# Kernel optimization log

Hardware: AMD Instinct MI355X
Metric: run time of the kernel (lower is better)

Reference implementation:

```python
import jax, jax.numpy as jnp
import numpy as np
import math

B, S, D, H = 2, 2048, 1024, 16
DH = D // H  # head_size = 64


def setup_inputs() -> dict:
    key = jax.random.key(0)
    ks = jax.random.split(key, 11)
    s = 0.02
    return {
        "queries": jax.random.normal(ks[0], (B, S, D), jnp.float32),
        "keys": jax.random.normal(ks[1], (B, S, D), jnp.float32),
        "values": jax.random.normal(ks[2], (B, S, D), jnp.float32),
        # nn.Linear weights: y = x @ W.T + b, W has shape (out, in)
        "W_Q": jax.random.normal(ks[3], (D, D), jnp.float32) * s,
        "b_Q": jax.random.normal(ks[4], (D,), jnp.float32) * s,
        "W_K": jax.random.normal(ks[5], (D, D), jnp.float32) * s,
        "b_K": jax.random.normal(ks[6], (D,), jnp.float32) * s,
        "W_V": jax.random.normal(ks[7], (D, D), jnp.float32) * s,
        "b_V": jax.random.normal(ks[8], (D,), jnp.float32) * s,
        "W_O": jax.random.normal(ks[9], (D, D), jnp.float32) * s,
        "b_O": jax.random.normal(ks[10], (D,), jnp.float32) * s,
    }


def _split_heads(x):
    # (B, S, H*DH) -> (B, H, S, DH); torch.chunk+stack == reshape+transpose
    b, s, _ = x.shape
    return x.reshape(b, s, H, DH).transpose(0, 2, 1, 3)


def reference(queries, keys, values, W_Q, b_Q, W_K, b_K, W_V, b_V, W_O, b_O):
    q = _split_heads(queries @ W_Q.T + b_Q)  # (B,H,S,DH)
    k = _split_heads(keys @ W_K.T + b_K)
    v = _split_heads(values @ W_V.T + b_V)

    scale = 1.0 / math.sqrt(DH)
    scores = jnp.einsum("bhqd,bhkd->bhqk", q, k) * scale  # (B,H,S,S)
    causal = jnp.tril(jnp.ones((S, S), dtype=bool))  # allow j <= i (causal)
    scores = jnp.where(causal, scores, -jnp.inf)
    weights = jax.nn.softmax(scores, axis=-1)

    attended = jnp.einsum("bhqk,bhkd->bhqd", weights, v)  # (B,H,S,DH)
    merged = attended.transpose(0, 2, 1, 3).reshape(B, S, D)  # merge_heads
    return merged @ W_O.T + b_O
```

## Files before the change

### kernel.cpp

```cpp
#include <hip/hip_runtime.h>


typedef __bf16 bf16x8 __attribute__((ext_vector_type(8)));
typedef float  f32x4  __attribute__((ext_vector_type(4)));

#define B_  2
#define S_  2048
#define D_  1024
#define H_  16
#define DH_ 64

#define NEG_ 1.0e30f
#define M2_  5.77078016f
#define QSCALE_ 0.18033688f

#if __has_builtin(__builtin_amdgcn_exp2f)
#define EXP2(x) __builtin_amdgcn_exp2f(x)
#else
#define EXP2(x) __builtin_exp2f(x)
#endif

__device__ __forceinline__ void load_lds16(const __bf16* g, __bf16* lds_base) {
    __builtin_amdgcn_global_load_lds(
        (const __attribute__((address_space(1))) void*)g,
        (__attribute__((address_space(3))) void*)lds_base,
        16, 0, 0);
}

__device__ __forceinline__ bf16x8 cvt8(const float* __restrict__ p) {
    const float4 a = *(const float4*)p;
    const float4 b = *(const float4*)(p + 4);
    bf16x8 r;
    r[0] = (__bf16)a.x; r[1] = (__bf16)a.y; r[2] = (__bf16)a.z; r[3] = (__bf16)a.w;
    r[4] = (__bf16)b.x; r[5] = (__bf16)b.y; r[6] = (__bf16)b.z; r[7] = (__bf16)b.w;
    return r;
}

__global__ void cvt_kernel(const float* __restrict__ q, const float* __restrict__ k,
                           const float* __restrict__ v,
                           const float* __restrict__ wq, const float* __restrict__ wk,
                           const float* __restrict__ wv, const float* __restrict__ wo,
                           __bf16* __restrict__ qb, __bf16* __restrict__ kb,
                           __bf16* __restrict__ vb,
                           __bf16* __restrict__ wqb, __bf16* __restrict__ wkb,
                           __bf16* __restrict__ wvb, __bf16* __restrict__ wob) {
    const int z = blockIdx.z;
    const float* src; __bf16* dst; size_t n;
    switch (z) {
        case 0: src = q;  dst = qb;  n = (size_t)B_ * S_ * D_; break;
        case 1: src = k;  dst = kb;  n = (size_t)B_ * S_ * D_; break;
        case 2: src = v;  dst = vb;  n = (size_t)B_ * S_ * D_; break;
        case 3: src = wq; dst = wqb; n = (size_t)D_ * D_; break;
        case 4: src = wk; dst = wkb; n = (size_t)D_ * D_; break;
        case 5: src = wv; dst = wvb; n = (size_t)D_ * D_; break;
        default: src = wo; dst = wob; n = (size_t)D_ * D_; break;
    }
    const size_t i = ((size_t)blockIdx.x * 256 + threadIdx.x) * 8;
    if (i >= n) return;
    *(bf16x8*)(dst + i) = cvt8(src + i);
}

__device__ __forceinline__ void gemm128_bf(const __bf16* __restrict__ X,
                                           const __bf16* __restrict__ W,
                                           int m0, int n0, int K,
                                           __bf16* As, __bf16* Bs,
                                           f32x4 acc[4][4]) {
    const int tid  = threadIdx.x;
    const int wave = tid >> 6, lane = tid & 63;
    const int row  = lane & 15, quad = lane >> 4;
    const int wm   = wave >> 1, wn = wave & 1;
    const int arow = lane >> 2;
    const int acol = (lane & 3) * 8;

    const f32x4 fzero = {0.f, 0.f, 0.f, 0.f};
#pragma unroll
    for (int mt = 0; mt < 4; ++mt)
#pragma unroll
        for (int nt = 0; nt < 4; ++nt) acc[mt][nt] = fzero;

    for (int k0 = 0; k0 < K; k0 += 32) {
#pragma unroll
        for (int c = 0; c < 2; ++c) {
            const int j = wave * 2 + c;
            load_lds16(X + (size_t)(m0 + j * 16 + arow) * K + k0 + acol, As + j * 512);
            load_lds16(W + (size_t)(n0 + j * 16 + arow) * K + k0 + acol, Bs + j * 512);
        }
        __syncthreads();
        bf16x8 af[4], bfv[4];
#pragma unroll
        for (int t = 0; t < 4; ++t) {
            af[t]  = *(const bf16x8*)(As + (wm * 64 + t * 16 + row) * 32 + quad * 8);
            bfv[t] = *(const bf16x8*)(Bs + (wn * 64 + t * 16 + row) * 32 + quad * 8);
        }
#pragma unroll
        for (int mt = 0; mt < 4; ++mt)
#pragma unroll
            for (int nt = 0; nt < 4; ++nt)
                acc[mt][nt] = __builtin_amdgcn_mfma_f32_16x16x32_bf16(
                    af[mt], bfv[nt], acc[mt][nt], 0, 0, 0);
        __syncthreads();
    }
}

__global__ void qkv_kernel(const __bf16* __restrict__ qb, const __bf16* __restrict__ kb,
                           const __bf16* __restrict__ vb,
                           const __bf16* __restrict__ wqb, const __bf16* __restrict__ wkb,
                           const __bf16* __restrict__ wvb,
                           const float* __restrict__ bq, const float* __restrict__ bk,
                           const float* __restrict__ bv,
                           __bf16* __restrict__ q_ws, __bf16* __restrict__ k_ws,
                           __bf16* __restrict__ v_ws) {
    __shared__ __align__(16) __bf16 As[128 * 32];
    __shared__ __align__(16) __bf16 Bs[128 * 32];
    const int mode = blockIdx.z;
    const __bf16* X    = mode == 0 ? qb : mode == 1 ? kb : vb;
    const __bf16* W    = mode == 0 ? wqb : mode == 1 ? wkb : wvb;
    const float*  bias = mode == 0 ? bq : mode == 1 ? bk : bv;
    const int m0 = blockIdx.y * 128, n0 = blockIdx.x * 128;

    f32x4 acc[4][4];
    gemm128_bf(X, W, m0, n0, D_, As, Bs, acc);

    const int tid = threadIdx.x;
    const int wave = tid >> 6, lane = tid & 63;
    const int row = lane & 15, quad = lane >> 4;
    const int wm = wave >> 1, wn = wave & 1;

#pragma unroll
    for (int nt = 0; nt < 4; ++nt) {
        const int n  = n0 + wn * 64 + nt * 16 + row;
        const float bf = bias[n];
        const int h = n >> 6, dh = n & 63;
#pragma unroll
        for (int mt = 0; mt < 4; ++mt) {
#pragma unroll
            for (int r = 0; r < 4; ++r) {
                const int m = m0 + wm * 64 + mt * 16 + quad * 4 + r;
                const int bb = m >> 11, s = m & (S_ - 1);
                const float val = acc[mt][nt][r] + bf;
                if (mode == 0)
                    q_ws[(((size_t)bb * H_ + h) * S_ + s) * DH_ + dh] = (__bf16)(val * QSCALE_);
                else if (mode == 1)
                    k_ws[(((size_t)bb * H_ + h) * S_ + s) * DH_ + dh] = (__bf16)val;
                else
                    v_ws[(((size_t)bb * H_ + h) * DH_ + dh) * S_ + s] = (__bf16)val;
            }
        }
    }
}

__global__ __launch_bounds__(256, 4)
void attn_kernel(const __bf16* __restrict__ q_ws, const __bf16* __restrict__ k_ws,
                 const __bf16* __restrict__ v_ws, __bf16* __restrict__ att) {
    __shared__ __align__(16) __bf16 Ks[128 * 64];
    __shared__ __align__(16) __bf16 Vs[64 * 128];
    __shared__ __align__(16) __bf16 Ps[4 * 16 * 32];

    const int bh = blockIdx.x;
    const int qt = (S_ / 64 - 1) - blockIdx.y;
    const int tid = threadIdx.x, wave = tid >> 6, lane = tid & 63;
    const int row = lane & 15, quad = lane >> 4;

    const __bf16* Qg = q_ws + ((size_t)bh * S_ + qt * 64 + wave * 16) * DH_;
    const __bf16* Kg = k_ws + (size_t)bh * S_ * DH_;
    const __bf16* Vg = v_ws + (size_t)bh * DH_ * S_;
    __bf16* Pw = Ps + wave * 512;

    bf16x8 qf[2];
#pragma unroll
    for (int ks = 0; ks < 2; ++ks)
        qf[ks] = *(const bf16x8*)(Qg + row * DH_ + ks * 32 + quad * 8);

    bf16x8 onesf;
#pragma unroll
    for (int i = 0; i < 8; ++i) onesf[i] = (__bf16)1.0f;

    const f32x4 fzero = {0.f, 0.f, 0.f, 0.f};
    f32x4 oacc[4];
    f32x4 lacc;
#pragma unroll
    for (int dt = 0; dt < 4; ++dt) oacc[dt] = fzero;
    lacc = fzero;

    const int klsub = lane >> 3;
    const int kcol  = ((lane & 7) ^ klsub) * 8;
    const int nkv = (qt >> 1) + 1;

    for (int kv = 0; kv < nkv; ++kv) {
#pragma unroll
        for (int c = 0; c < 4; ++c) {
            const int ck = wave * 4 + c;
            const int krow = ck * 8 + klsub;
            load_lds16(Kg + (size_t)(kv * 128 + krow) * DH_ + kcol, Ks + ck * 512);
            const int vrow = ck * 4 + (lane >> 4);
            const int vcol = ((lane & 15) ^ (vrow & 7)) * 8;
            load_lds16(Vg + (size_t)vrow * S_ + kv * 128 + vcol, Vs + ck * 512);
        }
        __syncthreads();

        const bool diag = (kv == nkv - 1);
        const int kcend = diag ? ((qt & 1) ? 4 : 2) : 4;
        const int swz = (row & 7) << 3;

        for (int kc = 0; kc < kcend; ++kc) {
            f32x4 s[2];
            s[0] = fzero; s[1] = fzero;
            __builtin_amdgcn_s_setprio(1);
#pragma unroll
            for (int jn = 0; jn < 2; ++jn) {
                const int nt = kc * 2 + jn;
                const int kb = (nt * 16 + row) * 64 + quad * 8;
                bf16x8 kf0 = *(const bf16x8*)(Ks + (kb ^ swz));
                bf16x8 kf1 = *(const bf16x8*)(Ks + ((kb + 32) ^ swz));
                s[jn] = __builtin_amdgcn_mfma_f32_16x16x32_bf16(qf[0], kf0, s[jn], 0, 0, 0);
                s[jn] = __builtin_amdgcn_mfma_f32_16x16x32_bf16(qf[1], kf1, s[jn], 0, 0, 0);
            }
            __builtin_amdgcn_s_setprio(0);

            if (diag) {
                const int rbase = (qt & 1) * 64;
#pragma unroll
                for (int jn = 0; jn < 2; ++jn) {
                    const int cloc = kc * 32 + jn * 16 + row;
#pragma unroll
                    for (int r = 0; r < 4; ++r) {
                        const int rloc = rbase + wave * 16 + quad * 4 + r;
                        if (cloc > rloc) s[jn][r] = -NEG_;
                    }
                }
            }

#pragma unroll
            for (int r = 0; r < 4; ++r)
#pragma unroll
                for (int jn = 0; jn < 2; ++jn) {
                    const float p = EXP2(s[jn][r] - M2_);
                    Pw[(((quad * 4 + r) * 32) + jn * 16 + row) ^ (quad << 3)] = (__bf16)p;
                }

            bf16x8 pf = *(const bf16x8*)(Pw + ((row * 32 + quad * 8) ^ (((row >> 2) & 3) << 3)));
            __builtin_amdgcn_s_setprio(1);
#pragma unroll
            for (int dt = 0; dt < 4; ++dt) {
                const int vb = (dt * 16 + row) * 128 + kc * 32 + quad * 8;
                bf16x8 vf = *(const bf16x8*)(Vs + (vb ^ swz));
                oacc[dt] = __builtin_amdgcn_mfma_f32_16x16x32_bf16(pf, vf, oacc[dt], 0, 0, 0);
            }
            lacc = __builtin_amdgcn_mfma_f32_16x16x32_bf16(pf, onesf, lacc, 0, 0, 0);
            __builtin_amdgcn_s_setprio(0);
        }
        __syncthreads();
    }

    const int b = bh >> 4, h = bh & 15;
#pragma unroll
    for (int r = 0; r < 4; ++r) {
        const float inv = 1.f / lacc[r];
        const int s = qt * 64 + wave * 16 + quad * 4 + r;
#pragma unroll
        for (int dt = 0; dt < 4; ++dt) {
            att[((size_t)b * S_ + s) * D_ + h * DH_ + dt * 16 + row] =
                (__bf16)(oacc[dt][r] * inv);
        }
    }
}

__global__ void oproj_kernel(const __bf16* __restrict__ attn, const __bf16* __restrict__ wob,
                             const float* __restrict__ bo, float* __restrict__ out) {
    __shared__ __align__(16) __bf16 As[128 * 32];
    __shared__ __align__(16) __bf16 Bs[128 * 32];
    const int m0 = blockIdx.y * 128, n0 = blockIdx.x * 128;

    f32x4 acc[4][4];
    gemm128_bf(attn, wob, m0, n0, D_, As, Bs, acc);

    const int tid = threadIdx.x;
    const int wave = tid >> 6, lane = tid & 63;
    const int row = lane & 15, quad = lane >> 4;
    const int wm = wave >> 1, wn = wave & 1;

#pragma unroll
    for (int nt = 0; nt < 4; ++nt) {
        const int n = n0 + wn * 64 + nt * 16 + row;
        const float bf = bo[n];
#pragma unroll
        for (int mt = 0; mt < 4; ++mt) {
#pragma unroll
            for (int r = 0; r < 4; ++r) {
                const int m = m0 + wm * 64 + mt * 16 + quad * 4 + r;
                out[(size_t)m * D_ + n] = acc[mt][nt][r] + bf;
            }
        }
    }
}

extern "C" void kernel_launch(void* const* d_in, const int* in_sizes, int n_in,
                              void* d_out, int out_size, void* d_ws, size_t ws_size,
                              hipStream_t stream) {
    const float* q_in = (const float*)d_in[0];
    const float* k_in = (const float*)d_in[1];
    const float* v_in = (const float*)d_in[2];
    const float* wq   = (const float*)d_in[3];
    const float* bq   = (const float*)d_in[4];
    const float* wk   = (const float*)d_in[5];
    const float* bk   = (const float*)d_in[6];
    const float* wv   = (const float*)d_in[7];
    const float* bv   = (const float*)d_in[8];
    const float* wo   = (const float*)d_in[9];
    const float* bo   = (const float*)d_in[10];

    char* ws = (char*)d_ws;
    const size_t MB = 1024 * 1024;
    __bf16* qb   = (__bf16*)(ws);
    __bf16* kb   = (__bf16*)(ws + 8 * MB);
    __bf16* vb   = (__bf16*)(ws + 16 * MB);
    __bf16* wqb  = (__bf16*)(ws + 24 * MB);
    __bf16* wkb  = (__bf16*)(ws + 26 * MB);
    __bf16* wvb  = (__bf16*)(ws + 28 * MB);
    __bf16* wob  = (__bf16*)(ws + 30 * MB);
    __bf16* q_ws = (__bf16*)(ws + 32 * MB);
    __bf16* k_ws = (__bf16*)(ws + 40 * MB);
    __bf16* v_ws = (__bf16*)(ws + 48 * MB);
    __bf16* attb = qb;
    float*  out  = (float*)d_out;

    cvt_kernel<<<dim3(2048, 1, 7), 256, 0, stream>>>(
        q_in, k_in, v_in, wq, wk, wv, wo, qb, kb, vb, wqb, wkb, wvb, wob);
    qkv_kernel<<<dim3(D_ / 128, (B_ * S_) / 128, 3), 256, 0, stream>>>(
        qb, kb, vb, wqb, wkb, wvb, bq, bk, bv, q_ws, k_ws, v_ws);
    attn_kernel<<<dim3(B_ * H_, S_ / 64), 256, 0, stream>>>(q_ws, k_ws, v_ws, attb);
    oproj_kernel<<<dim3(D_ / 128, (B_ * S_) / 128), 256, 0, stream>>>(attb, wob, bo, out);
}
```

Baseline: 225.6 us.

## Double-buffer LDS staging in GEMM and attention, shrink KV tile, remap attention grid

Adds double-buffered LDS for both GEMM kernels and the attention kernel, so the next K-step or KV tile is prefetched while the current one is consumed, and drops the trailing barrier. The attention KV tile shrinks from 128 to 64 keys so the double buffer fits the same LDS budget and the diagonal handling simplifies. It also flattens the attention grid into a 1D launch that interleaves batch-heads across consecutive blocks while keeping the longest query tiles first. This costs more loop iterations and barriers per KV pass and doubles GEMM LDS use, which may reduce occupancy.

Result: no change. 224.3 us (-0.6%).

```diff
diff --git a/kernel.cpp b/kernel.cpp
--- a/kernel.cpp
+++ b/kernel.cpp
@@ -78,27 +78,39 @@
 #pragma unroll
         for (int nt = 0; nt < 4; ++nt) acc[mt][nt] = fzero;
 
-    for (int k0 = 0; k0 < K; k0 += 32) {
+    auto stage = [&](int buf, int k0) {
 #pragma unroll
         for (int c = 0; c < 2; ++c) {
             const int j = wave * 2 + c;
-            load_lds16(X + (size_t)(m0 + j * 16 + arow) * K + k0 + acol, As + j * 512);
-            load_lds16(W + (size_t)(n0 + j * 16 + arow) * K + k0 + acol, Bs + j * 512);
-        }
+            load_lds16(X + (size_t)(m0 + j * 16 + arow) * K + k0 + acol,
+                       As + buf * 4096 + j * 512);
+            load_lds16(W + (size_t)(n0 + j * 16 + arow) * K + k0 + acol,
+                       Bs + buf * 4096 + j * 512);
+        }
+    };
+
+    stage(0, 0);
+    int cur = 0;
+    for (int k0 = 0; k0 < K; k0 += 32) {
         __syncthreads();
+        if (k0 + 32 < K) stage(cur ^ 1, k0 + 32);
+        const __bf16* Ab = As + cur * 4096;
+        const __bf16* Bb = Bs + cur * 4096;
         bf16x8 af[4], bfv[4];
 #pragma unroll
         for (int t = 0; t < 4; ++t) {
-            af[t]  = *(const bf16x8*)(As + (wm * 64 + t * 16 + row) * 32 + quad * 8);
-            bfv[t] = *(const bf16x8*)(Bs + (wn * 64 + t * 16 + row) * 32 + quad * 8);
-        }
+            af[t]  = *(const bf16x8*)(Ab + (wm * 64 + t * 16 + row) * 32 + quad * 8);
+            bfv[t] = *(const bf16x8*)(Bb + (wn * 64 + t * 16 + row) * 32 + quad * 8);
+        }
+        __builtin_amdgcn_s_setprio(1);
 #pragma unroll
         for (int mt = 0; mt < 4; ++mt)
 #pragma unroll
             for (int nt = 0; nt < 4; ++nt)
                 acc[mt][nt] = __builtin_amdgcn_mfma_f32_16x16x32_bf16(
                     af[mt], bfv[nt], acc[mt][nt], 0, 0, 0);
-        __syncthreads();
+        __builtin_amdgcn_s_setprio(0);
+        cur ^= 1;
     }
 }
 
@@ -110,8 +122,8 @@
                            const float* __restrict__ bv,
                            __bf16* __restrict__ q_ws, __bf16* __restrict__ k_ws,
                            __bf16* __restrict__ v_ws) {
-    __shared__ __align__(16) __bf16 As[128 * 32];
-    __shared__ __align__(16) __bf16 Bs[128 * 32];
+    __shared__ __align__(16) __bf16 As[2 * 128 * 32];
+    __shared__ __align__(16) __bf16 Bs[2 * 128 * 32];
     const int mode = blockIdx.z;
     const __bf16* X    = mode == 0 ? qb : mode == 1 ? kb : vb;
     const __bf16* W    = mode == 0 ? wqb : mode == 1 ? wkb : wvb;
@@ -152,12 +164,13 @@
 __global__ __launch_bounds__(256, 4)
 void attn_kernel(const __bf16* __restrict__ q_ws, const __bf16* __restrict__ k_ws,
                  const __bf16* __restrict__ v_ws, __bf16* __restrict__ att) {
-    __shared__ __align__(16) __bf16 Ks[128 * 64];
-    __shared__ __align__(16) __bf16 Vs[64 * 128];
+    __shared__ __align__(16) __bf16 Ks[2 * 64 * 64];
+    __shared__ __align__(16) __bf16 Vs[2 * 64 * 64];
     __shared__ __align__(16) __bf16 Ps[4 * 16 * 32];
 
-    const int bh = blockIdx.x;
-    const int qt = (S_ / 64 - 1) - blockIdx.y;
+    const int id = blockIdx.x;
+    const int bh = (id & 7) * 4 + ((id >> 3) & 3);
+    const int qt = 31 - (id >> 5);
     const int tid = threadIdx.x, wave = tid >> 6, lane = tid & 63;
     const int row = lane & 15, quad = lane >> 4;
 
@@ -177,32 +190,37 @@
 
     const f32x4 fzero = {0.f, 0.f, 0.f, 0.f};
     f32x4 oacc[4];
-    f32x4 lacc;
+    f32x4 lacc = fzero;
 #pragma unroll
     for (int dt = 0; dt < 4; ++dt) oacc[dt] = fzero;
-    lacc = fzero;
-
-    const int klsub = lane >> 3;
-    const int kcol  = ((lane & 7) ^ klsub) * 8;
-    const int nkv = (qt >> 1) + 1;
-
+
+    const int srow = lane >> 3;
+    const int scol = ((lane & 7) ^ srow) * 8;
+    const int nkv = qt + 1;
+
+    auto stage = [&](int buf, int kv) {
+        __bf16* Kd = Ks + buf * 4096;
+        __bf16* Vd = Vs + buf * 4096;
+#pragma unroll
+        for (int c = 0; c < 2; ++c) {
+            const int ck = wave * 2 + c;
+            load_lds16(Kg + (size_t)(kv * 64 + ck * 8 + srow) * DH_ + scol, Kd + ck * 512);
+            load_lds16(Vg + (size_t)(ck * 8 + srow) * S_ + kv * 64 + scol, Vd + ck * 512);
+        }
+    };
+
+    stage(0, 0);
+    int cur = 0;
     for (int kv = 0; kv < nkv; ++kv) {
-#pragma unroll
-        for (int c = 0; c < 4; ++c) {
-            const int ck = wave * 4 + c;
-            const int krow = ck * 8 + klsub;
-            load_lds16(Kg + (size_t)(kv * 128 + krow) * DH_ + kcol, Ks + ck * 512);
-            const int vrow = ck * 4 + (lane >> 4);
-            const int vcol = ((lane & 15) ^ (vrow & 7)) * 8;
-            load_lds16(Vg + (size_t)vrow * S_ + kv * 128 + vcol, Vs + ck * 512);
-        }
         __syncthreads();
-
+        if (kv + 1 < nkv) stage(cur ^ 1, kv + 1);
         const bool diag = (kv == nkv - 1);
-        const int kcend = diag ? ((qt & 1) ? 4 : 2) : 4;
+        const __bf16* Kb = Ks + cur * 4096;
+        const __bf16* Vb = Vs + cur * 4096;
         const int swz = (row & 7) << 3;
 
-        for (int kc = 0; kc < kcend; ++kc) {
+#pragma unroll
+        for (int kc = 0; kc < 2; ++kc) {
             f32x4 s[2];
             s[0] = fzero; s[1] = fzero;
             __builtin_amdgcn_s_setprio(1);
@@ -210,21 +228,20 @@
             for (int jn = 0; jn < 2; ++jn) {
                 const int nt = kc * 2 + jn;
                 const int kb = (nt * 16 + row) * 64 + quad * 8;
-                bf16x8 kf0 = *(const bf16x8*)(Ks + (kb ^ swz));
-                bf16x8 kf1 = *(const bf16x8*)(Ks + ((kb + 32) ^ swz));
+                bf16x8 kf0 = *(const bf16x8*)(Kb + (kb ^ swz));
+                bf16x8 kf1 = *(const bf16x8*)(Kb + ((kb + 32) ^ swz));
                 s[jn] = __builtin_amdgcn_mfma_f32_16x16x32_bf16(qf[0], kf0, s[jn], 0, 0, 0);
                 s[jn] = __builtin_amdgcn_mfma_f32_16x16x32_bf16(qf[1], kf1, s[jn], 0, 0, 0);
             }
             __builtin_amdgcn_s_setprio(0);
 
             if (diag) {
-                const int rbase = (qt & 1) * 64;
 #pragma unroll
                 for (int jn = 0; jn < 2; ++jn) {
                     const int cloc = kc * 32 + jn * 16 + row;
 #pragma unroll
                     for (int r = 0; r < 4; ++r) {
-                        const int rloc = rbase + wave * 16 + quad * 4 + r;
+                        const int rloc = wave * 16 + quad * 4 + r;
                         if (cloc > rloc) s[jn][r] = -NEG_;
                     }
                 }
@@ -242,14 +259,14 @@
             __builtin_amdgcn_s_setprio(1);
 #pragma unroll
             for (int dt = 0; dt < 4; ++dt) {
-                const int vb = (dt * 16 + row) * 128 + kc * 32 + quad * 8;
-                bf16x8 vf = *(const bf16x8*)(Vs + (vb ^ swz));
+                const int vb = (dt * 16 + row) * 64 + kc * 32 + quad * 8;
+                bf16x8 vf = *(const bf16x8*)(Vb + (vb ^ swz));
                 oacc[dt] = __builtin_amdgcn_mfma_f32_16x16x32_bf16(pf, vf, oacc[dt], 0, 0, 0);
             }
             lacc = __builtin_amdgcn_mfma_f32_16x16x32_bf16(pf, onesf, lacc, 0, 0, 0);
             __builtin_amdgcn_s_setprio(0);
         }
-        __syncthreads();
+        cur ^= 1;
     }
 
     const int b = bh >> 4, h = bh & 15;
@@ -267,8 +284,8 @@
 
 __global__ void oproj_kernel(const __bf16* __restrict__ attn, const __bf16* __restrict__ wob,
                              const float* __restrict__ bo, float* __restrict__ out) {
-    __shared__ __align__(16) __bf16 As[128 * 32];
-    __shared__ __align__(16) __bf16 Bs[128 * 32];
+    __shared__ __align__(16) __bf16 As[2 * 128 * 32];
+    __shared__ __align__(16) __bf16 Bs[2 * 128 * 32];
     const int m0 = blockIdx.y * 128, n0 = blockIdx.x * 128;
 
     f32x4 acc[4][4];
@@ -328,6 +345,6 @@
         q_in, k_in, v_in, wq, wk, wv, wo, qb, kb, vb, wqb, wkb, wvb, wob);
     qkv_kernel<<<dim3(D_ / 128, (B_ * S_) / 128, 3), 256, 0, stream>>>(
         qb, kb, vb, wqb, wkb, wvb, bq, bk, bv, q_ws, k_ws, v_ws);
-    attn_kernel<<<dim3(B_ * H_, S_ / 64), 256, 0, stream>>>(q_ws, k_ws, v_ws, attb);
+    attn_kernel<<<dim3(32 * 32), 256, 0, stream>>>(q_ws, k_ws, v_ws, attb);
     oproj_kernel<<<dim3(D_ / 128, (B_ * S_) / 128), 256, 0, stream>>>(attb, wob, bo, out);
 }
```
